# Optimization experiments

Measured on AMD Instinct MI355X. Metric: run time of the kernel, lower is better.

## Reference

```python
import jax, jax.numpy as jnp
import numpy as np
from jax import lax

NPOINT = 1024
RADIUS = 0.3
NSAMPLE = 64


def setup_inputs() -> dict:
    key = jax.random.key(0)
    ks = jax.random.split(key, 8)
    B, N, C = 4, 16384, 3
    xyz = jax.random.normal(ks[0], (B, N, 3), dtype=jnp.float32)
    features = jax.random.normal(ks[1], (B, N, C), dtype=jnp.float32)
    W1 = jax.random.normal(ks[2], (64, 6), dtype=jnp.float32) / np.sqrt(6.0)
    b1 = jnp.zeros((64,), dtype=jnp.float32)
    W2 = jax.random.normal(ks[3], (64, 64), dtype=jnp.float32) / np.sqrt(64.0)
    b2 = jnp.zeros((64,), dtype=jnp.float32)
    W3 = jax.random.normal(ks[4], (128, 64), dtype=jnp.float32) / np.sqrt(64.0)
    b3 = jnp.zeros((128,), dtype=jnp.float32)
    return {"xyz": xyz, "features": features, "W1": W1, "b1": b1,
            "W2": W2, "b2": b2, "W3": W3, "b3": b3}


def _fps_single(xyz, npoint):
    """Furthest point sampling for one cloud (N,3) -> (npoint,) int32 indices.
    Matches CUDA FPS: start at index 0, iteratively pick the point furthest
    from the selected set (min-distance maximization)."""
    N = xyz.shape[0]

    def body(carry, _):
        mindist, last = carry
        d = jnp.sum((xyz - xyz[last]) ** 2, axis=-1)  # (N,)
        mindist = jnp.minimum(mindist, d)
        nxt = jnp.argmax(mindist).astype(jnp.int32)
        return (mindist, nxt), nxt

    init = (jnp.full((N,), 1e10, dtype=xyz.dtype), jnp.int32(0))
    _, rest = lax.scan(body, init, None, length=npoint - 1)
    return jnp.concatenate([jnp.zeros((1,), jnp.int32), rest])


def _ball_query(xyz, new_xyz, radius, nsample):
    """xyz (B,N,3), new_xyz (B,P,3) -> (B,P,nsample) int32 indices.
    Matches CUDA ball_query: first nsample points within radius (in index
    order), remaining slots padded with the first valid index."""
    N = xyz.shape[1]
    d2 = jnp.sum((new_xyz[:, :, None, :] - xyz[:, None, :, :]) ** 2, axis=-1)  # (B,P,N)
    inball = d2 < radius * radius
    order = jnp.where(inball, jnp.arange(N, dtype=jnp.int32), jnp.int32(N))
    # k smallest indices == top_k of negated order
    idx = -lax.top_k(-order, nsample)[0]  # (B,P,nsample), sorted ascending
    first = idx[..., :1]
    idx = jnp.where(idx < N, idx, first)   # pad with first valid index
    idx = jnp.where(idx < N, idx, 0)       # safety if no neighbor at all
    return idx


def reference(xyz, features, W1, b1, W2, b2, W3, b3):
    B, N, _ = xyz.shape
    # --- FPS + gather centers ---
    fps_idx = jax.vmap(lambda p: _fps_single(p, NPOINT))(xyz)       # (B,P)
    bidx = jnp.arange(B)[:, None]
    new_xyz = xyz[bidx, fps_idx]                                    # (B,P,3)
    # --- ball query + grouping (QueryAndGroup with use_xyz=True) ---
    idx = _ball_query(xyz, new_xyz, RADIUS, NSAMPLE)                # (B,P,S)
    bidx2 = jnp.arange(B)[:, None, None]
    grouped_xyz = xyz[bidx2, idx] - new_xyz[:, :, None, :]          # (B,P,S,3)
    grouped_feat = features[bidx2, idx]                             # (B,P,S,C)
    g = jnp.concatenate([grouped_xyz, grouped_feat], axis=-1)       # (B,P,S,3+C)
    g = jnp.transpose(g, (0, 3, 1, 2))                              # (B,Cin,P,S)
    # --- shared MLP: 1x1 conv2d + ReLU stack ---
    h = jax.nn.relu(jnp.einsum('oc,bcps->bops', W1, g) + b1[None, :, None, None])
    h = jax.nn.relu(jnp.einsum('oc,bcps->bops', W2, h) + b2[None, :, None, None])
    h = jax.nn.relu(jnp.einsum('oc,bcps->bops', W3, h) + b3[None, :, None, None])
    # --- max-pool over the neighbor (sample) dim ---
    new_features = jnp.max(h, axis=-1)                              # (B,128,P)
    return new_xyz, new_features
```

## Files before the change

kernel.cpp:

```cpp
#include <hip/hip_runtime.h>

#define N_PTS   16384
#define NPOINT  1024
#define NSAMPLE 64
#define R2 ((float)(0.3 * 0.3))

__global__ __launch_bounds__(1024, 1) void fps_kernel(
    const float* __restrict__ xyz, float* __restrict__ out_newxyz) {
    const int b = blockIdx.x;
    const int t = threadIdx.x;
    const float* X = xyz + (size_t)b * N_PTS * 3;

    float px[16], py[16], pz[16], md[16];
#pragma unroll
    for (int j = 0; j < 16; ++j) {
        int n = j * 1024 + t;
        px[j] = X[3 * n];
        py[j] = X[3 * n + 1];
        pz[j] = X[3 * n + 2];
        md[j] = 1e10f;
    }

    float lx = X[0], ly = X[1], lz = X[2];
    if (t == 0) {
        out_newxyz[b * NPOINT * 3 + 0] = lx;
        out_newxyz[b * NPOINT * 3 + 1] = ly;
        out_newxyz[b * NPOINT * 3 + 2] = lz;
    }

    __shared__ float s_val[16];
    __shared__ int   s_idx[16];

    for (int i = 1; i < NPOINT; ++i) {
        float bv = -1.0f;
        int   bi = 0;
#pragma unroll
        for (int j = 0; j < 16; ++j) {
            float dx = px[j] - lx, dy = py[j] - ly, dz = pz[j] - lz;
            float d = dx * dx + dy * dy + dz * dz;
            float m = fminf(md[j], d);
            md[j] = m;
            if (m > bv) { bv = m; bi = j * 1024 + t; }
        }
#pragma unroll
        for (int off = 32; off > 0; off >>= 1) {
            float ov = __shfl_xor(bv, off, 64);
            int   oi = __shfl_xor(bi, off, 64);
            if (ov > bv) { bv = ov; bi = oi; }
        }
        if ((t & 63) == 0) { s_val[t >> 6] = bv; s_idx[t >> 6] = bi; }
        __syncthreads();
        float fv = s_val[0];
        int   fi = s_idx[0];
#pragma unroll
        for (int k = 1; k < 16; ++k) {
            float v = s_val[k];
            int   ix = s_idx[k];
            if (v > fv) { fv = v; fi = ix; }
        }
        __syncthreads();
        lx = X[3 * fi];
        ly = X[3 * fi + 1];
        lz = X[3 * fi + 2];
        if (t == 0) {
            out_newxyz[b * NPOINT * 3 + 3 * i]     = lx;
            out_newxyz[b * NPOINT * 3 + 3 * i + 1] = ly;
            out_newxyz[b * NPOINT * 3 + 3 * i + 2] = lz;
        }
    }
}

__global__ __launch_bounds__(256, 2) void bq_mlp_kernel(
    const float* __restrict__ xyz, const float* __restrict__ feat,
    const float* __restrict__ W1, const float* __restrict__ b1,
    const float* __restrict__ W2, const float* __restrict__ b2,
    const float* __restrict__ W3, const float* __restrict__ b3,
    const float* __restrict__ newxyz, float* __restrict__ out) {
    const int wave = threadIdx.x >> 6;
    const int lane = threadIdx.x & 63;
    const int q = blockIdx.x * 4 + wave;
    const int b = q >> 10;
    const int p = q & 1023;
    const float* X = xyz  + (size_t)b * N_PTS * 3;
    const float* F = feat + (size_t)b * N_PTS * 3;

    const float cx = newxyz[3 * q], cy = newxyz[3 * q + 1], cz = newxyz[3 * q + 2];

    __shared__ float g[4][NSAMPLE][6];

    int count = 0;
    for (int base = 0; base < N_PTS; base += 64) {
        int n = base + lane;
        float x = X[3 * n], y = X[3 * n + 1], z = X[3 * n + 2];
        float dx = x - cx, dy = y - cy, dz = z - cz;
        float d2 = dx * dx + dy * dy + dz * dz;
        bool in = d2 < R2;
        unsigned long long mask = __ballot(in);
        int slot = count + __popcll(mask & ((1ull << lane) - 1ull));
        if (in && slot < NSAMPLE) {
            float fx = F[3 * n], fy = F[3 * n + 1], fz = F[3 * n + 2];
            g[wave][slot][0] = dx; g[wave][slot][1] = dy; g[wave][slot][2] = dz;
            g[wave][slot][3] = fx; g[wave][slot][4] = fy; g[wave][slot][5] = fz;
        }
        count += __popcll(mask);
        if (count >= NSAMPLE) break;
    }
    asm volatile("s_waitcnt lgkmcnt(0)" ::: "memory");
    if (count == 0) {
        float x = X[0], y = X[1], z = X[2];
        g[wave][lane][0] = x - cx; g[wave][lane][1] = y - cy; g[wave][lane][2] = z - cz;
        g[wave][lane][3] = F[0];   g[wave][lane][4] = F[1];   g[wave][lane][5] = F[2];
    } else if (lane >= count) {
        float v0 = g[wave][0][0], v1 = g[wave][0][1], v2 = g[wave][0][2];
        float v3 = g[wave][0][3], v4 = g[wave][0][4], v5 = g[wave][0][5];
        g[wave][lane][0] = v0; g[wave][lane][1] = v1; g[wave][lane][2] = v2;
        g[wave][lane][3] = v3; g[wave][lane][4] = v4; g[wave][lane][5] = v5;
    }
    asm volatile("s_waitcnt lgkmcnt(0)" ::: "memory");

    float gv[6];
#pragma unroll
    for (int k = 0; k < 6; ++k) gv[k] = g[wave][lane][k];

    float h1[64];
#pragma unroll
    for (int o = 0; o < 64; ++o) {
        float a = b1[o];
#pragma unroll
        for (int c = 0; c < 6; ++c) a += W1[o * 6 + c] * gv[c];
        h1[o] = fmaxf(a, 0.0f);
    }
    float h2[64];
#pragma unroll
    for (int o = 0; o < 64; ++o) {
        float a = b2[o];
#pragma unroll
        for (int c = 0; c < 64; ++c) a += W2[o * 64 + c] * h1[c];
        h2[o] = fmaxf(a, 0.0f);
    }
    float o0 = 0.0f, o1 = 0.0f;
#pragma unroll
    for (int o = 0; o < 128; ++o) {
        float a = b3[o];
#pragma unroll
        for (int c = 0; c < 64; ++c) a += W3[o * 64 + c] * h2[c];
        a = fmaxf(a, 0.0f);
#pragma unroll
        for (int off = 32; off > 0; off >>= 1) a = fmaxf(a, __shfl_xor(a, off, 64));
        if (lane == (o & 63)) { if (o < 64) o0 = a; else o1 = a; }
    }
    out[(size_t)b * 128 * NPOINT + (size_t)lane        * NPOINT + p] = o0;
    out[(size_t)b * 128 * NPOINT + (size_t)(lane + 64) * NPOINT + p] = o1;
}

extern "C" void kernel_launch(void* const* d_in, const int* in_sizes, int n_in,
                              void* d_out, int out_size, void* d_ws, size_t ws_size,
                              hipStream_t stream) {
    const float* xyz  = (const float*)d_in[0];
    const float* feat = (const float*)d_in[1];
    const float* W1   = (const float*)d_in[2];
    const float* b1   = (const float*)d_in[3];
    const float* W2   = (const float*)d_in[4];
    const float* b2   = (const float*)d_in[5];
    const float* W3   = (const float*)d_in[6];
    const float* b3   = (const float*)d_in[7];
    float* out = (float*)d_out;

    float* out_newxyz = out;
    float* out_feat   = out + 4 * NPOINT * 3;

    fps_kernel<<<4, 1024, 0, stream>>>(xyz, out_newxyz);
    bq_mlp_kernel<<<1024, 256, 0, stream>>>(xyz, feat, W1, b1, W2, b2, W3, b3,
                                            out_newxyz, out_feat);
}
```

Baseline: 2.571 ms.

## Restructure FPS argmax as value-only reduction and remap MLP lanes to channels

The FPS loop now reduces only the maximum distance across the block, then resolves the winning index with an LDS atomicMin among threads holding that value. This drops the paired index shuffles and the serial index scan. The MLP stage is remapped so each lane owns an output channel and loops over samples. Weights sit in registers and activations are staged in shared memory, which replaces the per-output wave shuffle max-reduction with a per-lane running max. The cost is more registers and shared memory, plus an extra atomic and barrier per FPS iteration.

After: 2.082 ms. 1.24x faster.

```diff
diff --git a/kernel.cpp b/kernel.cpp
--- a/kernel.cpp
+++ b/kernel.cpp
@@ -9,7 +9,7 @@
     const float* __restrict__ xyz, float* __restrict__ out_newxyz) {
     const int b = blockIdx.x;
     const int t = threadIdx.x;
-    const float* X = xyz + (size_t)b * N_PTS * 3;
+    const float* __restrict__ X = xyz + (size_t)b * N_PTS * 3;
 
     float px[16], py[16], pz[16], md[16];
 #pragma unroll
@@ -21,51 +21,57 @@
         md[j] = 1e10f;
     }
 
+    __shared__ __align__(16) float s_val[16];
+    __shared__ int s_win[2];
+    if (t == 0) { s_win[0] = 0x7fffffff; s_win[1] = 0x7fffffff; }
+
     float lx = X[0], ly = X[1], lz = X[2];
     if (t == 0) {
         out_newxyz[b * NPOINT * 3 + 0] = lx;
         out_newxyz[b * NPOINT * 3 + 1] = ly;
         out_newxyz[b * NPOINT * 3 + 2] = lz;
     }
-
-    __shared__ float s_val[16];
-    __shared__ int   s_idx[16];
+    __syncthreads();
 
     for (int i = 1; i < NPOINT; ++i) {
-        float bv = -1.0f;
-        int   bi = 0;
+        float tv = -1.0f;
 #pragma unroll
         for (int j = 0; j < 16; ++j) {
             float dx = px[j] - lx, dy = py[j] - ly, dz = pz[j] - lz;
             float d = dx * dx + dy * dy + dz * dz;
             float m = fminf(md[j], d);
             md[j] = m;
-            if (m > bv) { bv = m; bi = j * 1024 + t; }
-        }
-#pragma unroll
-        for (int off = 32; off > 0; off >>= 1) {
-            float ov = __shfl_xor(bv, off, 64);
-            int   oi = __shfl_xor(bi, off, 64);
-            if (ov > bv) { bv = ov; bi = oi; }
-        }
-        if ((t & 63) == 0) { s_val[t >> 6] = bv; s_idx[t >> 6] = bi; }
+            tv = fmaxf(tv, m);
+        }
+        float wv = tv;
+#pragma unroll
+        for (int off = 32; off > 0; off >>= 1)
+            wv = fmaxf(wv, __shfl_xor(wv, off, 64));
+        if ((t & 63) == 0) s_val[t >> 6] = wv;
         __syncthreads();
-        float fv = s_val[0];
-        int   fi = s_idx[0];
-#pragma unroll
-        for (int k = 1; k < 16; ++k) {
-            float v = s_val[k];
-            int   ix = s_idx[k];
-            if (v > fv) { fv = v; fi = ix; }
+        const float4* sv4 = reinterpret_cast<const float4*>(s_val);
+        float4 a0 = sv4[0], a1 = sv4[1], a2 = sv4[2], a3 = sv4[3];
+        float f0 = fmaxf(fmaxf(a0.x, a0.y), fmaxf(a0.z, a0.w));
+        float f1 = fmaxf(fmaxf(a1.x, a1.y), fmaxf(a1.z, a1.w));
+        float f2 = fmaxf(fmaxf(a2.x, a2.y), fmaxf(a2.z, a2.w));
+        float f3 = fmaxf(fmaxf(a3.x, a3.y), fmaxf(a3.z, a3.w));
+        float fv = fmaxf(fmaxf(f0, f1), fmaxf(f2, f3));
+        if (tv == fv) {
+            int cand = 0x7fffffff;
+#pragma unroll
+            for (int j = 15; j >= 0; --j)
+                cand = (md[j] == fv) ? (j * 1024 + t) : cand;
+            atomicMin(&s_win[i & 1], cand);
         }
         __syncthreads();
-        lx = X[3 * fi];
-        ly = X[3 * fi + 1];
-        lz = X[3 * fi + 2];
+        int fi = s_win[i & 1];
+        if (t == 0) s_win[(i & 1) ^ 1] = 0x7fffffff;
+        int fis = __builtin_amdgcn_readfirstlane(fi);
+        const float* __restrict__ Xw = X + 3 * fis;
+        lx = Xw[0]; ly = Xw[1]; lz = Xw[2];
         if (t == 0) {
-            out_newxyz[b * NPOINT * 3 + 3 * i]     = lx;
-            out_newxyz[b * NPOINT * 3 + 3 * i + 1] = ly;
-            out_newxyz[b * NPOINT * 3 + 3 * i + 2] = lz;
+            float* o = out_newxyz + b * NPOINT * 3 + 3 * i;
+            o[0] = lx; o[1] = ly; o[2] = lz;
         }
     }
 }
@@ -81,12 +87,19 @@
     const int q = blockIdx.x * 4 + wave;
     const int b = q >> 10;
     const int p = q & 1023;
-    const float* X = xyz  + (size_t)b * N_PTS * 3;
-    const float* F = feat + (size_t)b * N_PTS * 3;
+    const float* __restrict__ X = xyz  + (size_t)b * N_PTS * 3;
+    const float* __restrict__ F = feat + (size_t)b * N_PTS * 3;
 
     const float cx = newxyz[3 * q], cy = newxyz[3 * q + 1], cz = newxyz[3 * q + 2];
 
-    __shared__ float g[4][NSAMPLE][6];
+    __shared__ __align__(16) float g[4][NSAMPLE][8];
+    __shared__ __align__(16) float h[4][NSAMPLE][64];
+
+    float w1r[6];
+#pragma unroll
+    for (int k = 0; k < 6; ++k) w1r[k] = W1[lane * 6 + k];
+    const float b1r = b1[lane];
+    const float b2r = b2[lane];
 
     int count = 0;
     for (int base = 0; base < N_PTS; base += 64) {
@@ -98,9 +111,9 @@
         unsigned long long mask = __ballot(in);
         int slot = count + __popcll(mask & ((1ull << lane) - 1ull));
         if (in && slot < NSAMPLE) {
-            float fx = F[3 * n], fy = F[3 * n + 1], fz = F[3 * n + 2];
             g[wave][slot][0] = dx; g[wave][slot][1] = dy; g[wave][slot][2] = dz;
-            g[wave][slot][3] = fx; g[wave][slot][4] = fy; g[wave][slot][5] = fz;
+            g[wave][slot][3] = F[3 * n]; g[wave][slot][4] = F[3 * n + 1];
+            g[wave][slot][5] = F[3 * n + 2];
         }
         count += __popcll(mask);
         if (count >= NSAMPLE) break;
@@ -116,41 +129,83 @@
         g[wave][lane][0] = v0; g[wave][lane][1] = v1; g[wave][lane][2] = v2;
         g[wave][lane][3] = v3; g[wave][lane][4] = v4; g[wave][lane][5] = v5;
     }
-    asm volatile("s_waitcnt lgkmcnt(0)" ::: "memory");
-
-    float gv[6];
-#pragma unroll
-    for (int k = 0; k < 6; ++k) gv[k] = g[wave][lane][k];
-
-    float h1[64];
-#pragma unroll
-    for (int o = 0; o < 64; ++o) {
-        float a = b1[o];
-#pragma unroll
-        for (int c = 0; c < 6; ++c) a += W1[o * 6 + c] * gv[c];
-        h1[o] = fmaxf(a, 0.0f);
-    }
-    float h2[64];
-#pragma unroll
-    for (int o = 0; o < 64; ++o) {
-        float a = b2[o];
-#pragma unroll
-        for (int c = 0; c < 64; ++c) a += W2[o * 64 + c] * h1[c];
-        h2[o] = fmaxf(a, 0.0f);
-    }
-    float o0 = 0.0f, o1 = 0.0f;
-#pragma unroll
-    for (int o = 0; o < 128; ++o) {
-        float a = b3[o];
-#pragma unroll
-        for (int c = 0; c < 64; ++c) a += W3[o * 64 + c] * h2[c];
-        a = fmaxf(a, 0.0f);
-#pragma unroll
-        for (int off = 32; off > 0; off >>= 1) a = fmaxf(a, __shfl_xor(a, off, 64));
-        if (lane == (o & 63)) { if (o < 64) o0 = a; else o1 = a; }
-    }
-    out[(size_t)b * 128 * NPOINT + (size_t)lane        * NPOINT + p] = o0;
-    out[(size_t)b * 128 * NPOINT + (size_t)(lane + 64) * NPOINT + p] = o1;
+    __syncthreads();
+
+    for (int s = 0; s < NSAMPLE; ++s) {
+        const float4* g4 = reinterpret_cast<const float4*>(&g[wave][s][0]);
+        float4 ga = g4[0], gb = g4[1];
+        float a = fmaf(w1r[0], ga.x, b1r);
+        a = fmaf(w1r[1], ga.y, a);
+        a = fmaf(w1r[2], ga.z, a);
+        a = fmaf(w1r[3], ga.w, a);
+        a = fmaf(w1r[4], gb.x, a);
+        a = fmaf(w1r[5], gb.y, a);
+        h[wave][s][lane] = fmaxf(a, 0.0f);
+    }
+    __syncthreads();
+
+    float w2r[64];
+    {
+        const float4* w4 = reinterpret_cast<const float4*>(W2 + (size_t)lane * 64);
+#pragma unroll
+        for (int cc = 0; cc < 16; ++cc) *reinterpret_cast<float4*>(&w2r[4 * cc]) = w4[cc];
+    }
+
+#pragma unroll 2
+    for (int s = 0; s < NSAMPLE; ++s) {
+        float a0 = 0.f, a1 = 0.f, a2 = 0.f, a3 = 0.f;
+        const float4* h4 = reinterpret_cast<const float4*>(&h[wave][s][0]);
+#pragma unroll
+        for (int cc = 0; cc < 16; ++cc) {
+            float4 hv = h4[cc];
+            a0 = fmaf(w2r[4 * cc + 0], hv.x, a0);
+            a1 = fmaf(w2r[4 * cc + 1], hv.y, a1);
+            a2 = fmaf(w2r[4 * cc + 2], hv.z, a2);
+            a3 = fmaf(w2r[4 * cc + 3], hv.w, a3);
+        }
+        float v = fmaxf(b2r + ((a0 + a1) + (a2 + a3)), 0.0f);
+        h[wave][s][lane] = v;
+    }
+    __syncthreads();
+
+    float w3a[64], w3b[64];
+    {
+        const float4* wa = reinterpret_cast<const float4*>(W3 + (size_t)lane * 64);
+        const float4* wb = reinterpret_cast<const float4*>(W3 + (size_t)(lane + 64) * 64);
+#pragma unroll
+        for (int cc = 0; cc < 16; ++cc) {
+            *reinterpret_cast<float4*>(&w3a[4 * cc]) = wa[cc];
+            *reinterpret_cast<float4*>(&w3b[4 * cc]) = wb[cc];
+        }
+    }
+    const float b3r0 = b3[lane];
+    const float b3r1 = b3[lane + 64];
+
+    float m0 = 0.0f, m1 = 0.0f;
+#pragma unroll 2
+    for (int s = 0; s < NSAMPLE; ++s) {
+        float a0 = 0.f, a1 = 0.f, a2 = 0.f, a3 = 0.f;
+        float c0 = 0.f, c1 = 0.f, c2 = 0.f, c3 = 0.f;
+        const float4* h4 = reinterpret_cast<const float4*>(&h[wave][s][0]);
+#pragma unroll
+        for (int cc = 0; cc < 16; ++cc) {
+            float4 hv = h4[cc];
+            a0 = fmaf(w3a[4 * cc + 0], hv.x, a0);
+            a1 = fmaf(w3a[4 * cc + 1], hv.y, a1);
+            a2 = fmaf(w3a[4 * cc + 2], hv.z, a2);
+            a3 = fmaf(w3a[4 * cc + 3], hv.w, a3);
+            c0 = fmaf(w3b[4 * cc + 0], hv.x, c0);
+            c1 = fmaf(w3b[4 * cc + 1], hv.y, c1);
+            c2 = fmaf(w3b[4 * cc + 2], hv.z, c2);
+            c3 = fmaf(w3b[4 * cc + 3], hv.w, c3);
+        }
+        float v0 = fmaxf(b3r0 + ((a0 + a1) + (a2 + a3)), 0.0f);
+        float v1 = fmaxf(b3r1 + ((c0 + c1) + (c2 + c3)), 0.0f);
+        m0 = fmaxf(m0, v0);
+        m1 = fmaxf(m1, v1);
+    }
+    out[(size_t)b * 128 * NPOINT + (size_t)lane        * NPOINT + p] = m0;
+    out[(size_t)b * 128 * NPOINT + (size_t)(lane + 64) * NPOINT + p] = m1;
 }
 
 extern "C" void kernel_launch(void* const* d_in, const int* in_sizes, int n_in,
```
